# Kernel optimization log

Measured on AMD Instinct MI355X. Metric: run time of the kernel, lower is better.

Reference implementation:

```python
import jax, jax.numpy as jnp
import numpy as np

DIM = 384
HEADS = 12
HEAD_DIM = DIM // HEADS
WS = 7            # window size
SHIFT = 3         # shift size
MLP_HIDDEN = int(DIM * 4.0)
SCALE = HEAD_DIM ** -0.5
N = WS * WS       # tokens per window


def _rel_pos_index():
    # identical to the torch buffer construction
    coords = np.stack(np.meshgrid(np.arange(WS), np.arange(WS), indexing='ij')).reshape(2, -1)
    rel = coords[:, :, None] - coords[:, None, :]          # (2, N, N)
    rel = rel.transpose(1, 2, 0).copy()                    # (N, N, 2)
    rel[:, :, 0] += WS - 1
    rel[:, :, 1] += WS - 1
    rel[:, :, 0] *= 2 * WS - 1
    return rel.sum(-1)                                      # (N, N) int

_REL_IDX = _rel_pos_index()


def _attn_mask_np(H, W):
    # shift mask, computed statically in numpy (H, W are Python ints)
    img = np.zeros((H, W), dtype=np.float32)
    cnt = 0
    for hs in (slice(0, -WS), slice(-WS, -SHIFT), slice(-SHIFT, None)):
        for ws_ in (slice(0, -WS), slice(-WS, -SHIFT), slice(-SHIFT, None)):
            img[hs, ws_] = cnt
            cnt += 1
    mw = img.reshape(H // WS, WS, W // WS, WS).transpose(0, 2, 1, 3).reshape(-1, N)  # (nW, N)
    diff = mw[:, None, :] - mw[:, :, None]                   # (nW, N, N)
    return np.where(diff != 0, np.float32(-100.0), np.float32(0.0))


def _layernorm(x, gamma, beta, eps=1e-5):
    mu = jnp.mean(x, axis=-1, keepdims=True)
    var = jnp.var(x, axis=-1, keepdims=True)
    return (x - mu) * jax.lax.rsqrt(var + eps) * gamma + beta


def setup_inputs() -> dict:
    key = jax.random.key(0)
    ks = jax.random.split(key, 8)
    B, H, W = 32, 56, 56
    s = 0.02
    return {
        'x': jax.random.normal(ks[0], (B, H * W, DIM), jnp.float32),
        'gamma1': jnp.ones((DIM,), jnp.float32),
        'beta1': jnp.zeros((DIM,), jnp.float32),
        'w_qkv': jax.random.normal(ks[1], (DIM, 3 * DIM), jnp.float32) * s,
        'b_qkv': jnp.zeros((3 * DIM,), jnp.float32),
        'rel_table': jax.random.normal(ks[2], ((2 * WS - 1) ** 2, HEADS), jnp.float32) * s,
        'w_proj': jax.random.normal(ks[3], (DIM, DIM), jnp.float32) * s,
        'b_proj': jnp.zeros((DIM,), jnp.float32),
        'gamma2': jnp.ones((DIM,), jnp.float32),
        'beta2': jnp.zeros((DIM,), jnp.float32),
        'w_fc1': jax.random.normal(ks[4], (DIM, MLP_HIDDEN), jnp.float32) * s,
        'b_fc1': jnp.zeros((MLP_HIDDEN,), jnp.float32),
        'w_fc2': jax.random.normal(ks[5], (MLP_HIDDEN, DIM), jnp.float32) * s,
        'b_fc2': jnp.zeros((DIM,), jnp.float32),
        'H': 56,
        'W': 56,
    }


def reference(x, gamma1, beta1, w_qkv, b_qkv, rel_table, w_proj, b_proj,
              gamma2, beta2, w_fc1, b_fc1, w_fc2, b_fc2, H, W):
    B, L, C = x.shape
    assert L == H * W and H % WS == 0 and W % WS == 0
    nWh, nWw = H // WS, W // WS
    nW = nWh * nWw

    shortcut = x
    h = _layernorm(x, gamma1, beta1).reshape(B, H, W, C)

    # cyclic shift
    h = jnp.roll(h, shift=(-SHIFT, -SHIFT), axis=(1, 2))

    # window partition -> (B*nW, N, C)
    h = h.reshape(B, nWh, WS, nWw, WS, C).transpose(0, 1, 3, 2, 4, 5).reshape(B * nW, N, C)

    # qkv
    qkv = (h @ w_qkv + b_qkv).reshape(B * nW, N, 3, HEADS, HEAD_DIM)
    q = qkv[:, :, 0].transpose(0, 2, 1, 3) * SCALE   # (B_, heads, N, d)
    k = qkv[:, :, 1].transpose(0, 2, 1, 3)
    v = qkv[:, :, 2].transpose(0, 2, 1, 3)

    attn = jnp.einsum('bhnd,bhmd->bhnm', q, k)       # (B_, heads, N, N)
    rel_bias = rel_table[_REL_IDX.reshape(-1)].reshape(N, N, HEADS).transpose(2, 0, 1)
    attn = attn + rel_bias[None]

    # shift mask (shift_size > 0)
    mask = jnp.asarray(_attn_mask_np(H, W))          # (nW, N, N)
    attn = attn.reshape(B, nW, HEADS, N, N) + mask[None, :, None]
    attn = jax.nn.softmax(attn.reshape(B * nW, HEADS, N, N), axis=-1)

    out = jnp.einsum('bhnm,bhmd->bhnd', attn, v).transpose(0, 2, 1, 3).reshape(B * nW, N, C)
    out = out @ w_proj + b_proj

    # window reverse -> (B, H, W, C)
    out = out.reshape(B, nWh, nWw, WS, WS, C).transpose(0, 1, 3, 2, 4, 5).reshape(B, H, W, C)
    out = jnp.roll(out, shift=(SHIFT, SHIFT), axis=(1, 2)).reshape(B, H * W, C)

    h = shortcut + out
    m = _layernorm(h, gamma2, beta2)
    m = jax.nn.gelu(m @ w_fc1 + b_fc1, approximate=False) @ w_fc2 + b_fc2
    return h + m
```

## Files before the change

### kernel.cpp

```cpp
#include <hip/hip_runtime.h>


#define DIMC   384
#define HEADS  12
#define HDIM   32
#define WSZ    7
#define SHIFTS 3
#define NTOK   49
#define HID    1536
#define BATCH  32
#define HH     56
#define WW2    56
#define NW     64
#define NWIN   (BATCH*NW)
#define TOK    (NWIN*NTOK)
#define QKSCALE 0.17677669529663687f

#define NCHUNK 4
#define ROWS_PER_CHUNK (TOK/NCHUNK)
#define WIN_PER_CHUNK  (NWIN/NCHUNK)

typedef short bf16x8 __attribute__((ext_vector_type(8)));
typedef float f32x4 __attribute__((ext_vector_type(4)));
typedef unsigned short ushort8_t __attribute__((ext_vector_type(8)));

__device__ __forceinline__ unsigned short f2bf(float f) {
  unsigned int u = __builtin_bit_cast(unsigned int, f);
  u += 0x7fffu + ((u >> 16) & 1u);
  return (unsigned short)(u >> 16);
}
__device__ __forceinline__ float bf2f(unsigned short s) {
  unsigned int u = ((unsigned int)s) << 16;
  return __builtin_bit_cast(float, u);
}

__device__ __forceinline__ float wave_sum(float v) {
#pragma unroll
  for (int o = 32; o > 0; o >>= 1) v += __shfl_xor(v, o, 64);
  return v;
}

__global__ __launch_bounds__(256) void transpose_cvt_kernel(
    const float* __restrict__ W, unsigned short* __restrict__ Wt, int K, int N) {
  __shared__ float t[32][33];
  int k0 = blockIdx.x * 32, n0 = blockIdx.y * 32;
  int tx = threadIdx.x & 31, ty = threadIdx.x >> 5;
#pragma unroll
  for (int i = 0; i < 4; i++) {
    int k = ty + i * 8;
    t[k][tx] = W[(size_t)(k0 + k) * N + n0 + tx];
  }
  __syncthreads();
#pragma unroll
  for (int i = 0; i < 4; i++) {
    int n = ty + i * 8;
    Wt[(size_t)(n0 + n) * K + k0 + tx] = f2bf(t[tx][n]);
  }
}

__global__ __launch_bounds__(256) void bias_precompute_kernel(
    const float* __restrict__ rel, float* __restrict__ combined) {
  int idx = blockIdx.x * 256 + threadIdx.x;
  int kt = idx & 63, qt = (idx >> 6) & 63;
  int hc = idx >> 12;
  int h = hc % 12, cls = hc / 12;
  float v;
  if (kt >= NTOK) v = -30000.f;
  else if (qt >= NTOK) v = 0.f;
  else {
    int yq = qt / 7, xq = qt % 7, yk = kt / 7, xk = kt % 7;
    v = rel[((yq - yk + 6) * 13 + (xq - xk + 6)) * HEADS + h];
    int wy7 = cls >> 1, wx7 = cls & 1;
    int rq = (wy7 ? (yq < 4 ? 1 : 2) : 0) * 3 + (wx7 ? (xq < 4 ? 1 : 2) : 0);
    int rk = (wy7 ? (yk < 4 ? 1 : 2) : 0) * 3 + (wx7 ? (xk < 4 ? 1 : 2) : 0);
    if (rq != rk) v -= 100.f;
  }
  combined[idx] = v;
}

__global__ __launch_bounds__(256) void ln1_window_kernel(
    const float* __restrict__ x, const float* __restrict__ gamma,
    const float* __restrict__ beta, unsigned short* __restrict__ out) {
  int wave = threadIdx.x >> 6, lane = threadIdx.x & 63;
  int token = blockIdx.x * 4 + wave;
  if (token >= TOK) return;
  int n  = token % NTOK;
  int b_ = token / NTOK;
  int b  = b_ >> 6;
  int w  = b_ & 63;
  int yw = (w >> 3) * WSZ + n / WSZ;
  int xw = (w & 7) * WSZ + n % WSZ;
  int ys = yw + SHIFTS; if (ys >= HH)  ys -= HH;
  int xs = xw + SHIFTS; if (xs >= WW2) xs -= WW2;
  const float* src = x + (size_t)(b * HH * WW2 + ys * WW2 + xs) * DIMC;
  float v[6], s = 0.f, s2 = 0.f;
#pragma unroll
  for (int i = 0; i < 6; i++) {
    v[i] = src[lane + 64 * i];
    s += v[i]; s2 += v[i] * v[i];
  }
  s = wave_sum(s); s2 = wave_sum(s2);
  float mu = s * (1.f / DIMC);
  float var = s2 * (1.f / DIMC) - mu * mu;
  float r = rsqrtf(var + 1e-5f);
  unsigned short* dst = out + (size_t)token * DIMC;
#pragma unroll
  for (int i = 0; i < 6; i++) {
    int c = lane + 64 * i;
    dst[c] = f2bf((v[i] - mu) * r * gamma[c] + beta[c]);
  }
}

template <bool GELU_ACT, bool ADD_SRC, bool OUT_BF16>
__global__ __launch_bounds__(256) void gemm_bf16_kernel(
    const unsigned short* __restrict__ A, const unsigned short* __restrict__ Bt,
    const float* __restrict__ bias, const float* __restrict__ addsrc,
    void* __restrict__ C, int M, int N, int K) {
  __shared__ unsigned short As[128][72];
  __shared__ unsigned short Bs[128][72];
  int tid = threadIdx.x;
  int lane = tid & 63, wid = tid >> 6;
  int wm = wid >> 1, wn = wid & 1;
  int bm0 = blockIdx.x * 128, bn0 = blockIdx.y * 128;

  f32x4 acc[4][4];
#pragma unroll
  for (int m = 0; m < 4; m++)
#pragma unroll
    for (int n = 0; n < 4; n++) acc[m][n] = (f32x4){0.f, 0.f, 0.f, 0.f};

  const unsigned short* Ab = A + (size_t)bm0 * K;
  const unsigned short* Bb = Bt + (size_t)bn0 * K;

  for (int k0 = 0; k0 < K; k0 += 64) {
#pragma unroll
    for (int it = 0; it < 4; it++) {
      int idx = tid + it * 256;
      int row = idx >> 3, seg = idx & 7;
      *(ushort8_t*)&As[row][seg * 8] =
          *(const ushort8_t*)(Ab + (size_t)row * K + k0 + seg * 8);
      *(ushort8_t*)&Bs[row][seg * 8] =
          *(const ushort8_t*)(Bb + (size_t)row * K + k0 + seg * 8);
    }
    __syncthreads();
#pragma unroll
    for (int kk = 0; kk < 2; kk++) {
      bf16x8 af[4], bfr[4];
      int kof = kk * 32 + (lane >> 4) * 8;
#pragma unroll
      for (int m = 0; m < 4; m++)
        af[m] = *(const bf16x8*)&As[wm * 64 + m * 16 + (lane & 15)][kof];
#pragma unroll
      for (int n = 0; n < 4; n++)
        bfr[n] = *(const bf16x8*)&Bs[wn * 64 + n * 16 + (lane & 15)][kof];
#pragma unroll
      for (int m = 0; m < 4; m++)
#pragma unroll
        for (int n = 0; n < 4; n++)
          acc[m][n] = __builtin_amdgcn_mfma_f32_16x16x32_bf16(
              af[m], bfr[n], acc[m][n], 0, 0, 0);
    }
    __syncthreads();
  }

#pragma unroll
  for (int n = 0; n < 4; n++) {
    int col = bn0 + wn * 64 + n * 16 + (lane & 15);
    float bb = bias[col];
#pragma unroll
    for (int m = 0; m < 4; m++) {
      int rowb = bm0 + wm * 64 + m * 16 + ((lane >> 4) << 2);
#pragma unroll
      for (int i = 0; i < 4; i++) {
        float v = acc[m][n][i] + bb;
        if (GELU_ACT) v = 0.5f * v * (1.f + erff(v * 0.70710678118f));
        size_t off = (size_t)(rowb + i) * N + col;
        if (ADD_SRC) v += addsrc[off];
        if (OUT_BF16) ((unsigned short*)C)[off] = f2bf(v);
        else          ((float*)C)[off] = v;
      }
    }
  }
}

__global__ __launch_bounds__(256) void attn_mfma_kernel(
    const unsigned short* __restrict__ qkv,
    const float* __restrict__ combined,
    unsigned short* __restrict__ ctx,
    int wbase) {
  __shared__ unsigned short Plds[4][64][64];
  __shared__ unsigned short Vt[4][32][64];
  __shared__ float rowsum[4][64];

  int wid = threadIdx.x >> 6, lane = threadIdx.x & 63;
  int gi = blockIdx.x * 4 + wid;
  int wl = gi / HEADS;
  int h  = gi % HEADS;
  int wg = wbase + wl;
  int w64 = wg & 63;
  int cls = (((w64 >> 3) == 7) ? 2 : 0) | (((w64 & 7) == 7) ? 1 : 0);
  const float* cmb = combined + ((size_t)(cls * HEADS + h) << 12);

  int q = lane & 15, g = lane >> 4;
  const unsigned short* base = qkv + (size_t)wl * NTOK * (3 * DIMC);
  const unsigned short* Qb = base + h * HDIM;
  const unsigned short* Kb = base + DIMC + h * HDIM;
  const unsigned short* Vb = base + 2 * DIMC + h * HDIM;

  unsigned short* pl = &Plds[wid][0][0];
  unsigned short* vt = &Vt[wid][0][0];

  {
    const unsigned short* vr = Vb + (size_t)lane * (3 * DIMC);
    ushort8_t vv[4];
#pragma unroll
    for (int j = 0; j < 4; j++) vv[j] = *(const ushort8_t*)(vr + j * 8);
#pragma unroll
    for (int j = 0; j < 4; j++)
#pragma unroll
      for (int e = 0; e < 8; e++) {
        int d = j * 8 + e;
        vt[d * 64 + (((lane >> 3) ^ (d & 7)) << 3) + (lane & 7)] = vv[j][e];
      }
  }

  bf16x8 kf[4];
#pragma unroll
  for (int mi = 0; mi < 4; mi++)
    kf[mi] = *(const bf16x8*)(Kb + (size_t)(16 * mi + q) * (3 * DIMC) + g * 8);

  const f32x4 zero4 = (f32x4){0.f, 0.f, 0.f, 0.f};
#pragma unroll
  for (int nj = 0; nj < 4; nj++) {
    bf16x8 qf = *(const bf16x8*)(Qb + (size_t)(16 * nj + q) * (3 * DIMC) + g * 8);
    f32x4 sa[4];
#pragma unroll
    for (int mi = 0; mi < 4; mi++)
      sa[mi] = __builtin_amdgcn_mfma_f32_16x16x32_bf16(kf[mi], qf, zero4, 0, 0, 0);
    int qt = 16 * nj + q;
    const float* cr = cmb + qt * 64;
    float mx = -1e30f;
#pragma unroll
    for (int mi = 0; mi < 4; mi++) {
      float4 bb = *(const float4*)&cr[16 * mi + 4 * g];
      sa[mi][0] = sa[mi][0] * QKSCALE + bb.x;
      sa[mi][1] = sa[mi][1] * QKSCALE + bb.y;
      sa[mi][2] = sa[mi][2] * QKSCALE + bb.z;
      sa[mi][3] = sa[mi][3] * QKSCALE + bb.w;
      mx = fmaxf(mx, fmaxf(fmaxf(sa[mi][0], sa[mi][1]), fmaxf(sa[mi][2], sa[mi][3])));
    }
    mx = fmaxf(mx, __shfl_xor(mx, 16, 64));
    mx = fmaxf(mx, __shfl_xor(mx, 32, 64));
    float sm = 0.f;
#pragma unroll
    for (int mi = 0; mi < 4; mi++)
#pragma unroll
      for (int i = 0; i < 4; i++) {
        float p = __expf(sa[mi][i] - mx);
        sa[mi][i] = p; sm += p;
      }
    sm += __shfl_xor(sm, 16, 64);
    sm += __shfl_xor(sm, 32, 64);
    if (g == 0) rowsum[wid][qt] = sm;
#pragma unroll
    for (int mi = 0; mi < 4; mi++) {
      int kt = 16 * mi + 4 * g;
      unsigned int lo = (unsigned int)f2bf(sa[mi][0]) | ((unsigned int)f2bf(sa[mi][1]) << 16);
      unsigned int hi = (unsigned int)f2bf(sa[mi][2]) | ((unsigned int)f2bf(sa[mi][3]) << 16);
      int idx = qt * 64 + (((kt >> 3) ^ (qt & 7)) << 3) + (kt & 7);
      uint2 pk; pk.x = lo; pk.y = hi;
      *(uint2*)&pl[idx] = pk;
    }
  }

  f32x4 pacc[4][2];
#pragma unroll
  for (int mi = 0; mi < 4; mi++)
#pragma unroll
    for (int nd = 0; nd < 2; nd++) pacc[mi][nd] = zero4;
#pragma unroll
  for (int kb = 0; kb < 2; kb++) {
    bf16x8 a[4], vfr[2];
#pragma unroll
    for (int mi = 0; mi < 4; mi++) {
      int row = 16 * mi + q;
      a[mi] = *(const bf16x8*)&pl[row * 64 + (((4 * kb + g) ^ (row & 7)) << 3)];
    }
#pragma unroll
    for (int nd = 0; nd < 2; nd++) {
      int row = 16 * nd + q;
      vfr[nd] = *(const bf16x8*)&vt[row * 64 + (((4 * kb + g) ^ (row & 7)) << 3)];
    }
#pragma unroll
    for (int mi = 0; mi < 4; mi++)
#pragma unroll
      for (int nd = 0; nd < 2; nd++)
        pacc[mi][nd] = __builtin_amdgcn_mfma_f32_16x16x32_bf16(
            a[mi], vfr[nd], pacc[mi][nd], 0, 0, 0);
  }

#pragma unroll
  for (int mi = 0; mi < 4; mi++)
#pragma unroll
    for (int i = 0; i < 4; i++) {
      int qt = 16 * mi + 4 * g + i;
      if (qt < NTOK) {
        float inv = 1.f / rowsum[wid][qt];
        size_t rowoff = ((size_t)wg * NTOK + qt) * DIMC + h * HDIM;
#pragma unroll
        for (int nd = 0; nd < 2; nd++)
          ctx[rowoff + 16 * nd + q] = f2bf(pacc[mi][nd][i] * inv);
      }
    }
}

__global__ __launch_bounds__(256) void unshift_ln2_kernel(
    const float* __restrict__ x, const unsigned short* __restrict__ projw,
    const float* __restrict__ gamma, const float* __restrict__ beta,
    float* __restrict__ hout, unsigned short* __restrict__ ln2) {
  int wave = threadIdx.x >> 6, lane = threadIdx.x & 63;
  int token = blockIdx.x * 4 + wave;
  if (token >= TOK) return;
  int b = token / (HH * WW2);
  int yx = token % (HH * WW2);
  int y = yx / WW2, xq = yx % WW2;
  int ys = y - SHIFTS;  if (ys < 0) ys += HH;
  int xs = xq - SHIFTS; if (xs < 0) xs += WW2;
  int wtok = (b * NW + (ys / WSZ) * 8 + (xs / WSZ)) * NTOK + (ys % WSZ) * WSZ + (xs % WSZ);
  const float* xp = x + (size_t)token * DIMC;
  const unsigned short* pp = projw + (size_t)wtok * DIMC;
  float v[6], s = 0.f, s2 = 0.f;
#pragma unroll
  for (int i = 0; i < 6; i++) {
    int c = lane + 64 * i;
    float hv = xp[c] + bf2f(pp[c]);
    v[i] = hv; s += hv; s2 += hv * hv;
  }
  s = wave_sum(s); s2 = wave_sum(s2);
  float mu = s * (1.f / DIMC);
  float var = s2 * (1.f / DIMC) - mu * mu;
  float r = rsqrtf(var + 1e-5f);
  float* hp = hout + (size_t)token * DIMC;
  unsigned short* lp = ln2 + (size_t)token * DIMC;
#pragma unroll
  for (int i = 0; i < 6; i++) {
    int c = lane + 64 * i;
    hp[c] = v[i];
    lp[c] = f2bf((v[i] - mu) * r * gamma[c] + beta[c]);
  }
}

extern "C" void kernel_launch(void* const* d_in, const int* in_sizes, int n_in,
                              void* d_out, int out_size, void* d_ws, size_t ws_size,
                              hipStream_t stream) {
  const float* x      = (const float*)d_in[0];
  const float* gamma1 = (const float*)d_in[1];
  const float* beta1  = (const float*)d_in[2];
  const float* w_qkv  = (const float*)d_in[3];
  const float* b_qkv  = (const float*)d_in[4];
  const float* rel_t  = (const float*)d_in[5];
  const float* w_proj = (const float*)d_in[6];
  const float* b_proj = (const float*)d_in[7];
  const float* gamma2 = (const float*)d_in[8];
  const float* beta2  = (const float*)d_in[9];
  const float* w_fc1  = (const float*)d_in[10];
  const float* b_fc1  = (const float*)d_in[11];
  const float* w_fc2  = (const float*)d_in[12];
  const float* b_fc2  = (const float*)d_in[13];

  char* p = (char*)d_ws;
  unsigned short* wqkvT = (unsigned short*)p; p += (size_t)1152 * 384 * 2;
  unsigned short* wprojT = (unsigned short*)p; p += (size_t)384 * 384 * 2;
  unsigned short* wfc1T = (unsigned short*)p; p += (size_t)1536 * 384 * 2;
  unsigned short* wfc2T = (unsigned short*)p; p += (size_t)384 * 1536 * 2;
  float* combined = (float*)p; p += (size_t)4 * 12 * 64 * 64 * 4;
  unsigned short* buf1 = (unsigned short*)p; p += (size_t)TOK * DIMC * 2;
  unsigned short* buf2 = (unsigned short*)p; p += (size_t)TOK * DIMC * 2;
  unsigned short* buf3 = (unsigned short*)p; p += (size_t)TOK * DIMC * 2;
  unsigned short* buf4 = (unsigned short*)p;
  float* out = (float*)d_out;

  transpose_cvt_kernel<<<dim3(384 / 32, 1152 / 32), 256, 0, stream>>>(w_qkv, wqkvT, 384, 1152);
  transpose_cvt_kernel<<<dim3(384 / 32, 384 / 32), 256, 0, stream>>>(w_proj, wprojT, 384, 384);
  transpose_cvt_kernel<<<dim3(384 / 32, 1536 / 32), 256, 0, stream>>>(w_fc1, wfc1T, 384, 1536);
  transpose_cvt_kernel<<<dim3(1536 / 32, 384 / 32), 256, 0, stream>>>(w_fc2, wfc2T, 1536, 384);
  bias_precompute_kernel<<<768, 256, 0, stream>>>(rel_t, combined);

  ln1_window_kernel<<<TOK / 4, 256, 0, stream>>>(x, gamma1, beta1, buf1);

  for (int c = 0; c < NCHUNK; c++) {
    const unsigned short* in = buf1 + (size_t)c * ROWS_PER_CHUNK * DIMC;
    gemm_bf16_kernel<false, false, true>
        <<<dim3(ROWS_PER_CHUNK / 128, 1152 / 128), 256, 0, stream>>>(
        in, wqkvT, b_qkv, nullptr, buf4, ROWS_PER_CHUNK, 3 * DIMC, DIMC);
    attn_mfma_kernel<<<WIN_PER_CHUNK * HEADS / 4, 256, 0, stream>>>(
        buf4, combined, buf2, c * WIN_PER_CHUNK);
  }

  gemm_bf16_kernel<false, false, true>
      <<<dim3(TOK / 128, DIMC / 128), 256, 0, stream>>>(
      buf2, wprojT, b_proj, nullptr, buf3, TOK, DIMC, DIMC);

  unshift_ln2_kernel<<<TOK / 4, 256, 0, stream>>>(x, buf3, gamma2, beta2, out, buf1);

  for (int c = 0; c < NCHUNK; c++) {
    const unsigned short* in = buf1 + (size_t)c * ROWS_PER_CHUNK * DIMC;
    float* hrow = out + (size_t)c * ROWS_PER_CHUNK * DIMC;
    gemm_bf16_kernel<true, false, true>
        <<<dim3(ROWS_PER_CHUNK / 128, HID / 128), 256, 0, stream>>>(
        in, wfc1T, b_fc1, nullptr, buf4, ROWS_PER_CHUNK, HID, DIMC);
    gemm_bf16_kernel<false, true, false>
        <<<dim3(ROWS_PER_CHUNK / 128, DIMC / 128), 256, 0, stream>>>(
        buf4, wfc2T, b_fc2, hrow, hrow, ROWS_PER_CHUNK, DIMC, HID);
  }
}
```

Before: 1.326 ms.

## Double-buffer GEMM tiles using direct global-to-LDS loads

The bf16 GEMM now stages tiles straight from global memory into LDS with global_load_lds and alternates between two LDS buffers, so the next K-tile is loaded while the current one feeds the MFMAs. The LDS padding is removed, which may bring back bank conflicts on the fragment reads. The chunk count used elsewhere drops from 4 to 2. Larger LDS use may lower occupancy, and nothing explicitly waits on the async loads beyond __syncthreads.

```diff
diff --git a/kernel.cpp b/kernel.cpp
--- a/kernel.cpp
+++ b/kernel.cpp
@@ -16,7 +16,7 @@
 #define TOK    (NWIN*NTOK)
 #define QKSCALE 0.17677669529663687f
 
-#define NCHUNK 4
+#define NCHUNK 2
 #define ROWS_PER_CHUNK (TOK/NCHUNK)
 #define WIN_PER_CHUNK  (NWIN/NCHUNK)
 
@@ -32,6 +32,13 @@
 __device__ __forceinline__ float bf2f(unsigned short s) {
   unsigned int u = ((unsigned int)s) << 16;
   return __builtin_bit_cast(float, u);
+}
+
+__device__ __forceinline__ void gload_lds16(const unsigned short* g,
+                                            unsigned short* lds_base_uniform) {
+  __builtin_amdgcn_global_load_lds(
+      (const __attribute__((address_space(1))) void*)g,
+      (__attribute__((address_space(3))) void*)lds_base_uniform, 16, 0, 0);
 }
 
 __device__ __forceinline__ float wave_sum(float v) {
@@ -111,13 +118,43 @@
   }
 }
 
+#define STAGE_TILE(AS, BS, K0)                                                \
+  {                                                                           \
+    for (int it = 0; it < 4; it++) {                                          \
+      int slot = it * 256 + wid * 64 + lane;                                  \
+      int row = slot >> 3, seg = slot & 7;                                    \
+      gload_lds16(Ab + (size_t)row * K + (K0) + seg * 8,                      \
+                  &AS[0][0] + (size_t)(it * 256 + wid * 64) * 8);             \
+      gload_lds16(Bb + (size_t)row * K + (K0) + seg * 8,                      \
+                  &BS[0][0] + (size_t)(it * 256 + wid * 64) * 8);             \
+    }                                                                         \
+  }
+
+#define COMPUTE_TILE(AS, BS)                                                  \
+  {                                                                           \
+    for (int kk = 0; kk < 2; kk++) {                                          \
+      bf16x8 af[4], bfr[4];                                                   \
+      int kof = kk * 32 + (lane >> 4) * 8;                                    \
+      for (int m = 0; m < 4; m++)                                             \
+        af[m] = *(const bf16x8*)&AS[wm * 64 + m * 16 + (lane & 15)][kof];     \
+      for (int n = 0; n < 4; n++)                                             \
+        bfr[n] = *(const bf16x8*)&BS[wn * 64 + n * 16 + (lane & 15)][kof];    \
+      for (int m = 0; m < 4; m++)                                             \
+        for (int n = 0; n < 4; n++)                                           \
+          acc[m][n] = __builtin_amdgcn_mfma_f32_16x16x32_bf16(                \
+              af[m], bfr[n], acc[m][n], 0, 0, 0);                             \
+    }                                                                         \
+  }
+
 template <bool GELU_ACT, bool ADD_SRC, bool OUT_BF16>
 __global__ __launch_bounds__(256) void gemm_bf16_kernel(
     const unsigned short* __restrict__ A, const unsigned short* __restrict__ Bt,
     const float* __restrict__ bias, const float* __restrict__ addsrc,
     void* __restrict__ C, int M, int N, int K) {
-  __shared__ unsigned short As[128][72];
-  __shared__ unsigned short Bs[128][72];
+  __shared__ unsigned short As0[128][64];
+  __shared__ unsigned short Bs0[128][64];
+  __shared__ unsigned short As1[128][64];
+  __shared__ unsigned short Bs1[128][64];
   int tid = threadIdx.x;
   int lane = tid & 63, wid = tid >> 6;
   int wm = wid >> 1, wn = wid & 1;
@@ -132,35 +169,19 @@
   const unsigned short* Ab = A + (size_t)bm0 * K;
   const unsigned short* Bb = Bt + (size_t)bn0 * K;
 
-  for (int k0 = 0; k0 < K; k0 += 64) {
-#pragma unroll
-    for (int it = 0; it < 4; it++) {
-      int idx = tid + it * 256;
-      int row = idx >> 3, seg = idx & 7;
-      *(ushort8_t*)&As[row][seg * 8] =
-          *(const ushort8_t*)(Ab + (size_t)row * K + k0 + seg * 8);
-      *(ushort8_t*)&Bs[row][seg * 8] =
-          *(const ushort8_t*)(Bb + (size_t)row * K + k0 + seg * 8);
-    }
+  const int nt = K >> 6;
+  STAGE_TILE(As0, Bs0, 0);
+  __syncthreads();
+
+  for (int t = 0; t < nt; t += 2) {
+    if (t + 1 < nt) STAGE_TILE(As1, Bs1, (t + 1) << 6);
+    COMPUTE_TILE(As0, Bs0);
     __syncthreads();
-#pragma unroll
-    for (int kk = 0; kk < 2; kk++) {
-      bf16x8 af[4], bfr[4];
-      int kof = kk * 32 + (lane >> 4) * 8;
-#pragma unroll
-      for (int m = 0; m < 4; m++)
-        af[m] = *(const bf16x8*)&As[wm * 64 + m * 16 + (lane & 15)][kof];
-#pragma unroll
-      for (int n = 0; n < 4; n++)
-        bfr[n] = *(const bf16x8*)&Bs[wn * 64 + n * 16 + (lane & 15)][kof];
-#pragma unroll
-      for (int m = 0; m < 4; m++)
-#pragma unroll
-        for (int n = 0; n < 4; n++)
-          acc[m][n] = __builtin_amdgcn_mfma_f32_16x16x32_bf16(
-              af[m], bfr[n], acc[m][n], 0, 0, 0);
-    }
-    __syncthreads();
+    if (t + 1 < nt) {
+      if (t + 2 < nt) STAGE_TILE(As0, Bs0, (t + 2) << 6);
+      COMPUTE_TILE(As1, Bs1);
+      __syncthreads();
+    }
   }
 
 #pragma unroll
```

Result: faster. 1.231 ms (-7.2%).
